# Performance work log

Hardware: AMD Instinct MI355X
Metric: run time of the kernel (lower is better)

## Reference

```python
import jax, jax.numpy as jnp
import numpy as np

N, E, P, H, O = 20000, 640000, 12, 128, 12


def setup_inputs() -> dict:
    key = jax.random.key(0)
    ks = jax.random.split(key, 18)
    s = 0.05
    return {
        "x": jax.random.normal(ks[0], (N, P), jnp.float32),
        "edge_index": jax.random.randint(ks[1], (2, E), 0, N, jnp.int32),
        "edge_weight": jax.random.uniform(ks[2], (E,), jnp.float32),
        "attention": jax.random.uniform(ks[3], (P,), jnp.float32),
        "conv_w_z": jax.random.normal(ks[4], (1, H), jnp.float32) * s,
        "conv_b_z": jnp.zeros((H,), jnp.float32),
        "lin_w_z": jax.random.normal(ks[5], (2 * H, H), jnp.float32) * s,
        "lin_b_z": jnp.zeros((H,), jnp.float32),
        "conv_w_r": jax.random.normal(ks[6], (1, H), jnp.float32) * s,
        "conv_b_r": jnp.zeros((H,), jnp.float32),
        "lin_w_r": jax.random.normal(ks[7], (2 * H, H), jnp.float32) * s,
        "lin_b_r": jnp.zeros((H,), jnp.float32),
        "conv_w_h": jax.random.normal(ks[8], (1, H), jnp.float32) * s,
        "conv_b_h": jnp.zeros((H,), jnp.float32),
        "lin_w_h": jax.random.normal(ks[9], (2 * H, H), jnp.float32) * s,
        "lin_b_h": jnp.zeros((H,), jnp.float32),
        "lin_out_w": jax.random.normal(ks[10], (H, O), jnp.float32) * s,
        "lin_out_b": jnp.zeros((O,), jnp.float32),
    }


def _gcn_norm(edge_index, edge_weight, n):
    # PyG gcn_norm with add_self_loops=True (fill_value 1.0)
    src, dst = edge_index[0], edge_index[1]
    loop = jnp.arange(n, dtype=src.dtype)
    src = jnp.concatenate([src, loop])
    dst = jnp.concatenate([dst, loop])
    w = jnp.concatenate([edge_weight, jnp.ones((n,), edge_weight.dtype)])
    deg = jax.ops.segment_sum(w, dst, num_segments=n)
    dinv = jnp.where(deg > 0.0, jax.lax.rsqrt(deg), 0.0)
    return src, dst, dinv[src] * w * dinv[dst]


def reference(x, edge_index, edge_weight, attention,
              conv_w_z, conv_b_z, lin_w_z, lin_b_z,
              conv_w_r, conv_b_r, lin_w_r, lin_b_r,
              conv_w_h, conv_b_h, lin_w_h, lin_b_h,
              lin_out_w, lin_out_b):
    # Dropout is identity in eval mode.
    n, p = x.shape
    hdim = lin_b_z.shape[0]
    src, dst, norm = _gcn_norm(edge_index, edge_weight, n)
    # GCN aggregation is linear in X; aggregate all periods at once: [N, P]
    agg = jax.ops.segment_sum(norm[:, None] * x[src], dst, num_segments=n)

    def conv(cw, cb):  # GCNConv with in_channels=1: [N,P] -> [N,P,H]
        return agg[:, :, None] * cw[0][None, None, :] + cb

    # A3TGCN calls TGCN with H=None every period -> hidden state is zeros,
    # so cat([conv_out, H]) @ W == conv_out @ W[:hdim], H*R == 0 (R has no
    # effect), and H_next = Z*H + (1-Z)*H_tilde == (1-Z)*H_tilde, exactly.
    Z = jax.nn.sigmoid(jnp.einsum('nph,hk->npk', conv(conv_w_z, conv_b_z), lin_w_z[:hdim]) + lin_b_z)
    H_tilde = jnp.tanh(jnp.einsum('nph,hk->npk', conv(conv_w_h, conv_b_h), lin_w_h[:hdim]) + lin_b_h)
    H_per = (1.0 - Z) * H_tilde  # [N, P, H]

    probs = jax.nn.softmax(attention)  # [P]
    h = jnp.einsum('p,nph->nh', probs, H_per)  # attention-weighted sum over periods
    h = jax.nn.elu(h)
    return h @ lin_out_w + lin_out_b
```

## Files before the change

### kernel.cpp

```cpp
#include <hip/hip_runtime.h>


#define PP 12
#define HH 128
#define OO 12
#define CAP 96

__device__ __forceinline__ void precompute_body(
    int k,
    const float* __restrict__ cwz, const float* __restrict__ cbz,
    const float* __restrict__ Wz, const float* __restrict__ lbz,
    const float* __restrict__ cwh, const float* __restrict__ cbh,
    const float* __restrict__ Wh, const float* __restrict__ lbh,
    const float* __restrict__ att,
    float* __restrict__ az, float* __restrict__ bz,
    float* __restrict__ ah, float* __restrict__ bh,
    float* __restrict__ probs) {
    float sz = 0.f, tz = 0.f, sh = 0.f, th = 0.f;
    for (int h = 0; h < HH; ++h) {
        float wz = Wz[h * HH + k];
        float wh = Wh[h * HH + k];
        sz += cwz[h] * wz;
        tz += cbz[h] * wz;
        sh += cwh[h] * wh;
        th += cbh[h] * wh;
    }
    az[k] = sz;
    bz[k] = tz + lbz[k];
    ah[k] = sh;
    bh[k] = th + lbh[k];
    if (k == 0) {
        float m = -1e30f;
        for (int p = 0; p < PP; ++p) m = fmaxf(m, att[p]);
        float e[PP], ssum = 0.f;
        for (int p = 0; p < PP; ++p) { e[p] = __expf(att[p] - m); ssum += e[p]; }
        float inv = 1.0f / ssum;
        for (int p = 0; p < PP; ++p) probs[p] = e[p] * inv;
    }
}

__global__ void k_init(int* __restrict__ zeroarr, int n,
                       const float* cwz, const float* cbz, const float* Wz, const float* lbz,
                       const float* cwh, const float* cbh, const float* Wh, const float* lbh,
                       const float* att,
                       float* az, float* bz, float* ah, float* bh, float* probs) {
    int i = blockIdx.x * blockDim.x + threadIdx.x;
    if (i < n) zeroarr[i] = 0;
    if (blockIdx.x == 0 && threadIdx.x < HH)
        precompute_body(threadIdx.x, cwz, cbz, Wz, lbz, cwh, cbh, Wh, lbh, att,
                        az, bz, ah, bh, probs);
}

__global__ void k_fill_bucket(const int* __restrict__ srcv, const int* __restrict__ dstv,
                              const float* __restrict__ ew, int* __restrict__ cursor,
                              int2* __restrict__ bucket, int e) {
    int i = blockIdx.x * blockDim.x + threadIdx.x;
    if (i >= e) return;
    int d = dstv[i];
    int pos = atomicAdd(&cursor[d], 1);
    if (pos < CAP) bucket[(long)d * CAP + pos] = make_int2(srcv[i], __float_as_int(ew[i]));
}

__global__ void k_hist(const int* __restrict__ dstv, int* __restrict__ count, int e) {
    int i = blockIdx.x * blockDim.x + threadIdx.x;
    if (i < e) atomicAdd(&count[dstv[i]], 1);
}

__global__ void __launch_bounds__(256) k_scan(const int* __restrict__ count,
                                              int* __restrict__ rowptr,
                                              int* __restrict__ cursor, int n) {
    __shared__ int s_sum[256];
    int t = threadIdx.x;
    int chunk = (n + 255) / 256;
    int lo = t * chunk, hi = min(n, lo + chunk);
    int s = 0;
    for (int i = lo; i < hi; ++i) s += count[i];
    s_sum[t] = s;
    __syncthreads();
    for (int off = 1; off < 256; off <<= 1) {
        int v = (t >= off) ? s_sum[t - off] : 0;
        __syncthreads();
        s_sum[t] += v;
        __syncthreads();
    }
    int run = (t == 0) ? 0 : s_sum[t - 1];
    for (int i = lo; i < hi; ++i) {
        rowptr[i] = run;
        cursor[i] = run;
        run += count[i];
    }
}

__global__ void k_fill_csr(const int* __restrict__ srcv, const int* __restrict__ dstv,
                           const float* __restrict__ ew, int* __restrict__ cursor,
                           int2* __restrict__ csr, int e) {
    int i = blockIdx.x * blockDim.x + threadIdx.x;
    if (i >= e) return;
    int d = dstv[i];
    int pos = atomicAdd(&cursor[d], 1);
    csr[pos] = make_int2(srcv[i], __float_as_int(ew[i]));
}

__global__ void __launch_bounds__(256) k_deg(const int* __restrict__ rowptr,
                                             const int* __restrict__ count, int cap,
                                             const int2* __restrict__ csr,
                                             float* __restrict__ dinv, int n) {
    int wid = (blockIdx.x * blockDim.x + threadIdx.x) >> 6;
    int lane = threadIdx.x & 63;
    if (wid >= n) return;
    long base = (cap > 0) ? (long)wid * cap : rowptr[wid];
    int len = count[wid];
    if (cap > 0) len = min(len, cap);
    float s = 0.f;
    for (int i = lane; i < len; i += 64) s += __int_as_float(csr[base + i].y);
#pragma unroll
    for (int off = 32; off > 0; off >>= 1) s += __shfl_xor(s, off, 64);
    if (lane == 0) dinv[wid] = rsqrtf(1.0f + s);
}

__global__ void __launch_bounds__(HH) k_fused(
    const int* __restrict__ rowptr, const int* __restrict__ count, int cap,
    const int2* __restrict__ csr, const float* __restrict__ dinv,
    const float* __restrict__ x,
    const float* __restrict__ az, const float* __restrict__ bz,
    const float* __restrict__ ah, const float* __restrict__ bh,
    const float* __restrict__ probs,
    const float* __restrict__ Wout, const float* __restrict__ bout,
    float* __restrict__ out, int n) {
    __shared__ float s_c[128];
    __shared__ int   s_src[128];
    __shared__ float s_part[PP][10];
    __shared__ float s_agg[PP], s_probs[PP], s_h[HH];
    int node = blockIdx.x;
    int t = threadIdx.x;
    float dv_n = dinv[node];
    long base = (cap > 0) ? (long)node * cap : rowptr[node];
    int len = count[node];
    if (cap > 0) len = min(len, cap);
    if (t < PP) s_probs[t] = probs[t];
    int p = t % PP, j = t / PP;
    float acc_g = (t < PP) ? dv_n * dv_n * x[(long)node * PP + t] : 0.f;
    if (t >= 120) acc_g = 0.f;
    for (int ch = 0; ch < len; ch += 128) {
        int clen = min(128, len - ch);
        __syncthreads();
        if (t < clen) {
            int2 sw = csr[base + ch + t];
            s_src[t] = sw.x;
            s_c[t] = dinv[sw.x] * __int_as_float(sw.y) * dv_n;
        }
        __syncthreads();
        if (t < 120)
            for (int i = j; i < clen; i += 10)
                acc_g += s_c[i] * x[(long)s_src[i] * PP + p];
    }
    if (t < 120) s_part[p][j] = acc_g;
    __syncthreads();
    if (t < PP) {
        float a = 0.f;
#pragma unroll
        for (int j2 = 0; j2 < 10; ++j2) a += s_part[t][j2];
        s_agg[t] = a;
    }
    __syncthreads();
    float a_z = az[t], b_z = bz[t], a_h = ah[t], b_h = bh[t];
    float acc = 0.0f;
#pragma unroll
    for (int q = 0; q < PP; ++q) {
        float g = s_agg[q];
        float omz = 1.0f / (1.0f + __expf(g * a_z + b_z));
        float y = g * a_h + b_h;
        y = fminf(fmaxf(y, -15.0f), 15.0f);
        float e2 = __expf(2.0f * y);
        float tnh = (e2 - 1.0f) / (e2 + 1.0f);
        acc += s_probs[q] * omz * tnh;
    }
    s_h[t] = acc > 0.0f ? acc : expm1f(acc);
    __syncthreads();
    if (t < OO) {
        float s = bout[t];
#pragma unroll 8
        for (int j2 = 0; j2 < HH; ++j2) s += s_h[j2] * Wout[j2 * OO + t];
        out[(long)node * OO + t] = s;
    }
}

extern "C" void kernel_launch(void* const* d_in, const int* in_sizes, int n_in,
                              void* d_out, int out_size, void* d_ws, size_t ws_size,
                              hipStream_t stream) {
    const float* x    = (const float*)d_in[0];
    const int*   ei   = (const int*)d_in[1];
    const float* ew   = (const float*)d_in[2];
    const float* att  = (const float*)d_in[3];
    const float* cwz  = (const float*)d_in[4];
    const float* cbz  = (const float*)d_in[5];
    const float* Wz   = (const float*)d_in[6];
    const float* lbz  = (const float*)d_in[7];
    const float* cwh  = (const float*)d_in[12];
    const float* cbh  = (const float*)d_in[13];
    const float* Wh   = (const float*)d_in[14];
    const float* lbh  = (const float*)d_in[15];
    const float* Wout = (const float*)d_in[16];
    const float* bout = (const float*)d_in[17];
    float* out = (float*)d_out;

    const int E = in_sizes[2];
    const int N = in_sizes[0] / PP;
    const int* srcv = ei;
    const int* dstv = ei + E;

    char* wsb = (char*)d_ws;
    size_t bucket_bytes = (size_t)N * CAP * sizeof(int2);
    size_t bucket_need = bucket_bytes + (size_t)N * 8 + (4 * HH + PP + 64) * 4;

    if (ws_size >= bucket_need) {
        int2*  bucket = (int2*)wsb;
        int*   cursor = (int*)(wsb + bucket_bytes);
        float* dinv   = (float*)(cursor + N);
        float* az     = dinv + N;
        float* bz     = az + HH;
        float* ah     = bz + HH;
        float* bh     = ah + HH;
        float* probs  = bh + HH;

        k_init<<<(N + 255) / 256, 256, 0, stream>>>(cursor, N,
            cwz, cbz, Wz, lbz, cwh, cbh, Wh, lbh, att, az, bz, ah, bh, probs);
        k_fill_bucket<<<(E + 255) / 256, 256, 0, stream>>>(srcv, dstv, ew, cursor, bucket, E);
        k_deg<<<((long)N * 64 + 255) / 256, 256, 0, stream>>>(nullptr, cursor, CAP, bucket, dinv, N);
        k_fused<<<N, HH, 0, stream>>>(nullptr, cursor, CAP, bucket, dinv, x,
                                      az, bz, ah, bh, probs, Wout, bout, out, N);
    } else {
        int2*  csr    = (int2*)wsb;
        int*   count  = (int*)(wsb + (size_t)E * sizeof(int2));
        int*   rowptr = count + N;
        int*   cursor = rowptr + N;
        float* dinv   = (float*)(cursor + N);
        float* az     = dinv + N;
        float* bz     = az + HH;
        float* ah     = bz + HH;
        float* bh     = ah + HH;
        float* probs  = bh + HH;

        k_init<<<(N + 255) / 256, 256, 0, stream>>>(count, N,
            cwz, cbz, Wz, lbz, cwh, cbh, Wh, lbh, att, az, bz, ah, bh, probs);
        k_hist<<<(E + 255) / 256, 256, 0, stream>>>(dstv, count, E);
        k_scan<<<1, 256, 0, stream>>>(count, rowptr, cursor, N);
        k_fill_csr<<<(E + 255) / 256, 256, 0, stream>>>(srcv, dstv, ew, cursor, csr, E);
        k_deg<<<((long)N * 64 + 255) / 256, 256, 0, stream>>>(rowptr, count, 0, csr, dinv, N);
        k_fused<<<N, HH, 0, stream>>>(rowptr, count, 0, csr, dinv, x,
                                      az, bz, ah, bh, probs, Wout, bout, out, N);
    }
}
```

Before: 187.0 us.

## Fold degree computation into bucket fill with atomics and drop separate degree kernel

The separate degree kernel is removed. Weighted degree is now accumulated with float atomics during bucket or CSR fill, and each consumer computes rsqrt(1+deg) on the fly. The init kernel is replaced by a memset, and the weight precompute moves into the last block of the fill kernel. The change also adds fast reciprocal intrinsics, packs source index and coefficient into a float2 in shared memory, and parallelises the output projection across 120 threads. The trade-off is extra float atomics during the fill, repeated rsqrt per edge, and float summation order that depends on atomic ordering.

```diff
diff --git a/kernel.cpp b/kernel.cpp
--- a/kernel.cpp
+++ b/kernel.cpp
@@ -5,6 +5,9 @@
 #define HH 128
 #define OO 12
 #define CAP 96
+
+__device__ __forceinline__ float fast_rcp(float x) { return __builtin_amdgcn_rcpf(x); }
+__device__ __forceinline__ float fast_rsq(float x) { return __builtin_amdgcn_rsqf(x); }
 
 __device__ __forceinline__ void precompute_body(
     int k,
@@ -39,31 +42,35 @@
     }
 }
 
-__global__ void k_init(int* __restrict__ zeroarr, int n,
+__global__ void k_fill(const int* __restrict__ srcv, const int* __restrict__ dstv,
+                       const float* __restrict__ ew, int* __restrict__ cursor,
+                       float* __restrict__ deg, int2* __restrict__ bucket, int e,
                        const float* cwz, const float* cbz, const float* Wz, const float* lbz,
                        const float* cwh, const float* cbh, const float* Wh, const float* lbh,
                        const float* att,
                        float* az, float* bz, float* ah, float* bh, float* probs) {
-    int i = blockIdx.x * blockDim.x + threadIdx.x;
-    if (i < n) zeroarr[i] = 0;
-    if (blockIdx.x == 0 && threadIdx.x < HH)
-        precompute_body(threadIdx.x, cwz, cbz, Wz, lbz, cwh, cbh, Wh, lbh, att,
-                        az, bz, ah, bh, probs);
-}
-
-__global__ void k_fill_bucket(const int* __restrict__ srcv, const int* __restrict__ dstv,
-                              const float* __restrict__ ew, int* __restrict__ cursor,
-                              int2* __restrict__ bucket, int e) {
+    if (blockIdx.x == gridDim.x - 1) {
+        if (threadIdx.x < HH)
+            precompute_body(threadIdx.x, cwz, cbz, Wz, lbz, cwh, cbh, Wh, lbh, att,
+                            az, bz, ah, bh, probs);
+        return;
+    }
     int i = blockIdx.x * blockDim.x + threadIdx.x;
     if (i >= e) return;
     int d = dstv[i];
+    float w = ew[i];
     int pos = atomicAdd(&cursor[d], 1);
-    if (pos < CAP) bucket[(long)d * CAP + pos] = make_int2(srcv[i], __float_as_int(ew[i]));
-}
-
-__global__ void k_hist(const int* __restrict__ dstv, int* __restrict__ count, int e) {
+    if (pos < CAP) bucket[(long)d * CAP + pos] = make_int2(srcv[i], __float_as_int(w));
+    atomicAdd(&deg[d], w);
+}
+
+__global__ void k_hist(const int* __restrict__ dstv, const float* __restrict__ ew,
+                       int* __restrict__ count, float* __restrict__ deg, int e) {
     int i = blockIdx.x * blockDim.x + threadIdx.x;
-    if (i < e) atomicAdd(&count[dstv[i]], 1);
+    if (i < e) {
+        atomicAdd(&count[dstv[i]], 1);
+        atomicAdd(&deg[dstv[i]], ew[i]);
+    }
 }
 
 __global__ void __launch_bounds__(256) k_scan(const int* __restrict__ count,
@@ -93,7 +100,17 @@
 
 __global__ void k_fill_csr(const int* __restrict__ srcv, const int* __restrict__ dstv,
                            const float* __restrict__ ew, int* __restrict__ cursor,
-                           int2* __restrict__ csr, int e) {
+                           int2* __restrict__ csr, int e,
+                           const float* cwz, const float* cbz, const float* Wz, const float* lbz,
+                           const float* cwh, const float* cbh, const float* Wh, const float* lbh,
+                           const float* att,
+                           float* az, float* bz, float* ah, float* bh, float* probs) {
+    if (blockIdx.x == gridDim.x - 1) {
+        if (threadIdx.x < HH)
+            precompute_body(threadIdx.x, cwz, cbz, Wz, lbz, cwh, cbh, Wh, lbh, att,
+                            az, bz, ah, bh, probs);
+        return;
+    }
     int i = blockIdx.x * blockDim.x + threadIdx.x;
     if (i >= e) return;
     int d = dstv[i];
@@ -101,58 +118,42 @@
     csr[pos] = make_int2(srcv[i], __float_as_int(ew[i]));
 }
 
-__global__ void __launch_bounds__(256) k_deg(const int* __restrict__ rowptr,
-                                             const int* __restrict__ count, int cap,
-                                             const int2* __restrict__ csr,
-                                             float* __restrict__ dinv, int n) {
-    int wid = (blockIdx.x * blockDim.x + threadIdx.x) >> 6;
-    int lane = threadIdx.x & 63;
-    if (wid >= n) return;
-    long base = (cap > 0) ? (long)wid * cap : rowptr[wid];
-    int len = count[wid];
-    if (cap > 0) len = min(len, cap);
-    float s = 0.f;
-    for (int i = lane; i < len; i += 64) s += __int_as_float(csr[base + i].y);
-#pragma unroll
-    for (int off = 32; off > 0; off >>= 1) s += __shfl_xor(s, off, 64);
-    if (lane == 0) dinv[wid] = rsqrtf(1.0f + s);
-}
-
 __global__ void __launch_bounds__(HH) k_fused(
     const int* __restrict__ rowptr, const int* __restrict__ count, int cap,
-    const int2* __restrict__ csr, const float* __restrict__ dinv,
+    const int2* __restrict__ csr, const float* __restrict__ deg,
     const float* __restrict__ x,
     const float* __restrict__ az, const float* __restrict__ bz,
     const float* __restrict__ ah, const float* __restrict__ bh,
     const float* __restrict__ probs,
     const float* __restrict__ Wout, const float* __restrict__ bout,
     float* __restrict__ out, int n) {
-    __shared__ float s_c[128];
-    __shared__ int   s_src[128];
+    __shared__ float2 s_cs[128];
     __shared__ float s_part[PP][10];
     __shared__ float s_agg[PP], s_probs[PP], s_h[HH];
     int node = blockIdx.x;
     int t = threadIdx.x;
-    float dv_n = dinv[node];
+    float dv_n = fast_rsq(1.0f + deg[node]);
     long base = (cap > 0) ? (long)node * cap : rowptr[node];
     int len = count[node];
     if (cap > 0) len = min(len, cap);
     if (t < PP) s_probs[t] = probs[t];
     int p = t % PP, j = t / PP;
-    float acc_g = (t < PP) ? dv_n * dv_n * x[(long)node * PP + t] : 0.f;
+    float acc_g = (t < PP) ? dv_n * dv_n * x[node * PP + t] : 0.f;
     if (t >= 120) acc_g = 0.f;
     for (int ch = 0; ch < len; ch += 128) {
         int clen = min(128, len - ch);
         __syncthreads();
         if (t < clen) {
             int2 sw = csr[base + ch + t];
-            s_src[t] = sw.x;
-            s_c[t] = dinv[sw.x] * __int_as_float(sw.y) * dv_n;
+            float c = __int_as_float(sw.y) * fast_rsq(1.0f + deg[sw.x]) * dv_n;
+            s_cs[t] = make_float2(c, __int_as_float(sw.x * PP));
         }
         __syncthreads();
         if (t < 120)
-            for (int i = j; i < clen; i += 10)
-                acc_g += s_c[i] * x[(long)s_src[i] * PP + p];
+            for (int i = j; i < clen; i += 10) {
+                float2 cs = s_cs[i];
+                acc_g += cs.x * x[__float_as_int(cs.y) + p];
+            }
     }
     if (t < 120) s_part[p][j] = acc_g;
     __syncthreads();
@@ -168,20 +169,26 @@
 #pragma unroll
     for (int q = 0; q < PP; ++q) {
         float g = s_agg[q];
-        float omz = 1.0f / (1.0f + __expf(g * a_z + b_z));
+        float omz = fast_rcp(1.0f + __expf(g * a_z + b_z));
         float y = g * a_h + b_h;
         y = fminf(fmaxf(y, -15.0f), 15.0f);
         float e2 = __expf(2.0f * y);
-        float tnh = (e2 - 1.0f) / (e2 + 1.0f);
+        float tnh = 1.0f - 2.0f * fast_rcp(e2 + 1.0f);
         acc += s_probs[q] * omz * tnh;
     }
     s_h[t] = acc > 0.0f ? acc : expm1f(acc);
+    __syncthreads();
+    if (t < 120) {
+        float s = 0.f;
+        for (int j2 = j; j2 < HH; j2 += 10) s += s_h[j2] * Wout[j2 * OO + p];
+        s_part[p][j] = s;
+    }
     __syncthreads();
     if (t < OO) {
         float s = bout[t];
-#pragma unroll 8
-        for (int j2 = 0; j2 < HH; ++j2) s += s_h[j2] * Wout[j2 * OO + t];
-        out[(long)node * OO + t] = s;
+#pragma unroll
+        for (int j2 = 0; j2 < 10; ++j2) s += s_part[t][j2];
+        out[node * OO + t] = s;
     }
 }
 
@@ -216,38 +223,36 @@
     if (ws_size >= bucket_need) {
         int2*  bucket = (int2*)wsb;
         int*   cursor = (int*)(wsb + bucket_bytes);
-        float* dinv   = (float*)(cursor + N);
-        float* az     = dinv + N;
+        float* deg    = (float*)(cursor + N);
+        float* az     = deg + N;
         float* bz     = az + HH;
         float* ah     = bz + HH;
         float* bh     = ah + HH;
         float* probs  = bh + HH;
 
-        k_init<<<(N + 255) / 256, 256, 0, stream>>>(cursor, N,
+        hipMemsetAsync(cursor, 0, (size_t)N * 2 * sizeof(int), stream);
+        k_fill<<<(E + 255) / 256 + 1, 256, 0, stream>>>(srcv, dstv, ew, cursor, deg, bucket, E,
             cwz, cbz, Wz, lbz, cwh, cbh, Wh, lbh, att, az, bz, ah, bh, probs);
-        k_fill_bucket<<<(E + 255) / 256, 256, 0, stream>>>(srcv, dstv, ew, cursor, bucket, E);
-        k_deg<<<((long)N * 64 + 255) / 256, 256, 0, stream>>>(nullptr, cursor, CAP, bucket, dinv, N);
-        k_fused<<<N, HH, 0, stream>>>(nullptr, cursor, CAP, bucket, dinv, x,
+        k_fused<<<N, HH, 0, stream>>>(nullptr, cursor, CAP, bucket, deg, x,
                                       az, bz, ah, bh, probs, Wout, bout, out, N);
     } else {
         int2*  csr    = (int2*)wsb;
         int*   count  = (int*)(wsb + (size_t)E * sizeof(int2));
-        int*   rowptr = count + N;
+        float* deg    = (float*)(count + N);
+        int*   rowptr = (int*)(deg + N);
         int*   cursor = rowptr + N;
-        float* dinv   = (float*)(cursor + N);
-        float* az     = dinv + N;
+        float* az     = (float*)(cursor + N);
         float* bz     = az + HH;
         float* ah     = bz + HH;
         float* bh     = ah + HH;
         float* probs  = bh + HH;
 
-        k_init<<<(N + 255) / 256, 256, 0, stream>>>(count, N,
+        hipMemsetAsync(count, 0, (size_t)N * 2 * sizeof(int), stream);
+        k_hist<<<(E + 255) / 256, 256, 0, stream>>>(dstv, ew, count, deg, E);
+        k_scan<<<1, 256, 0, stream>>>(count, rowptr, cursor, N);
+        k_fill_csr<<<(E + 255) / 256 + 1, 256, 0, stream>>>(srcv, dstv, ew, cursor, csr, E,
             cwz, cbz, Wz, lbz, cwh, cbh, Wh, lbh, att, az, bz, ah, bh, probs);
-        k_hist<<<(E + 255) / 256, 256, 0, stream>>>(dstv, count, E);
-        k_scan<<<1, 256, 0, stream>>>(count, rowptr, cursor, N);
-        k_fill_csr<<<(E + 255) / 256, 256, 0, stream>>>(srcv, dstv, ew, cursor, csr, E);
-        k_deg<<<((long)N * 64 + 255) / 256, 256, 0, stream>>>(rowptr, count, 0, csr, dinv, N);
-        k_fused<<<N, HH, 0, stream>>>(rowptr, count, 0, csr, dinv, x,
+        k_fused<<<N, HH, 0, stream>>>(rowptr, count, 0, csr, deg, x,
                                       az, bz, ah, bh, probs, Wout, bout, out, N);
     }
 }
```

New measurement: 190.4 us. Within noise of the previous version (+1.8%).
